# Optimization experiments

Measured on AMD Instinct MI355X. Metric: run time of the kernel, lower is better.

The kernel has to match this reference:

```python
import jax, jax.numpy as jnp
import numpy as np

B, S, D, T, H = 4, 2048, 1024, 5, 8


def setup_inputs() -> dict:
    key = jax.random.key(0)
    ks = jax.random.split(key, 12)
    sc = 0.02  # small init scale for weights so attention logits stay sane
    return {
        "x": jax.random.normal(ks[0], (B, S, D), jnp.float32),
        "time_steps": jax.random.randint(ks[1], (B, S), 0, T),
        "gamma": jnp.ones((T, D), jnp.float32),
        "beta": jax.random.normal(ks[2], (T, D), jnp.float32) * sc,
        "decay": jnp.ones((T,), jnp.float32),
        "shift_W": jax.random.normal(ks[3], (D, D), jnp.float32) * sc,
        "shift_b": jax.random.normal(ks[4], (D,), jnp.float32) * sc,
        "in_proj_W": jax.random.normal(ks[5], (3 * D, D), jnp.float32) * sc,
        "in_proj_b": jax.random.normal(ks[6], (3 * D,), jnp.float32) * sc,
        "out_proj_W": jax.random.normal(ks[7], (D, D), jnp.float32) * sc,
        "out_proj_b": jax.random.normal(ks[8], (D,), jnp.float32) * sc,
    }


def reference(x, time_steps, gamma, beta, decay, shift_W, shift_b,
              in_proj_W, in_proj_b, out_proj_W, out_proj_b):
    eps = 1e-5
    T_ = gamma.shape[0]
    b_, s_, d_ = x.shape
    hd = d_ // H

    # --- per-token indexed LayerNorm + decay (vectorized gather of norm params) ---
    idx = jnp.clip(time_steps, 0, T_ - 1)              # safe gather index [B,S]
    mu = jnp.mean(x, axis=-1, keepdims=True)
    var = jnp.mean(jnp.square(x - mu), axis=-1, keepdims=True)
    xn = (x - mu) * jax.lax.rsqrt(var + eps)           # [B,S,D]
    normed = (xn * gamma[idx] + beta[idx]) * decay[idx][..., None]
    x = jnp.where((time_steps < T_)[..., None], normed, x)

    # --- residual temporal shift (Linear) ---
    x = x + x @ shift_W.T + shift_b

    # --- torch-style MultiheadAttention(x, x, x), batch_first ---
    qkv = x @ in_proj_W.T + in_proj_b                  # [B,S,3D]
    q, k, v = jnp.split(qkv, 3, axis=-1)
    q = q.reshape(b_, s_, H, hd)
    k = k.reshape(b_, s_, H, hd)
    v = v.reshape(b_, s_, H, hd)
    scale = 1.0 / jnp.sqrt(jnp.asarray(hd, x.dtype))
    scores = jnp.einsum('bqhd,bkhd->bhqk', q, k) * scale   # [B,H,S,S]
    attn = jax.nn.softmax(scores, axis=-1)
    ctx = jnp.einsum('bhqk,bkhd->bqhd', attn, v).reshape(b_, s_, d_)
    attended = ctx @ out_proj_W.T + out_proj_b
    return x + attended
```

## Files before the change

kernel.cpp:

```cpp
#include <hip/hip_runtime.h>
#include <math.h>

#define B_ 4
#define S_ 2048
#define D_ 1024
#define T_ 5
#define H_ 8
#define HD_ 128
#define M_ (B_*S_)

typedef __bf16 bf16x8 __attribute__((ext_vector_type(8)));
typedef float  f32x4  __attribute__((ext_vector_type(4)));

__device__ __forceinline__ float bf2f(unsigned short u) {
    union { unsigned int i; float f; } c; c.i = ((unsigned int)u) << 16; return c.f;
}
__device__ __forceinline__ unsigned short f2bf(float f) {
    __bf16 h = (__bf16)f;
    unsigned short u; __builtin_memcpy(&u, &h, 2); return u;
}

__device__ __forceinline__ void gll16(const void* g, void* l) {
    __builtin_amdgcn_global_load_lds(
        (const __attribute__((address_space(1))) void*)g,
        (__attribute__((address_space(3))) void*)l, 16, 0, 0);
}

__global__ __launch_bounds__(256) void f2bf_kernel(
    const float* __restrict__ src, unsigned short* __restrict__ dst)
{
    int i = (blockIdx.x * 256 + threadIdx.x) * 4;
    float4 v = *(const float4*)(src + i);
    ushort4 o;
    o.x = f2bf(v.x); o.y = f2bf(v.y); o.z = f2bf(v.z); o.w = f2bf(v.w);
    *(ushort4*)(dst + i) = o;
}

__global__ __launch_bounds__(256) void ln_kernel(
    const float* __restrict__ x, const int* __restrict__ ts,
    const float* __restrict__ gamma, const float* __restrict__ beta,
    const float* __restrict__ decay, unsigned short* __restrict__ out)
{
    int row = blockIdx.x;
    int tid = threadIdx.x;
    float4 v = ((const float4*)(x + (size_t)row * D_))[tid];
    float s  = v.x + v.y + v.z + v.w;
    float s2 = v.x*v.x + v.y*v.y + v.z*v.z + v.w*v.w;
    #pragma unroll
    for (int off = 32; off; off >>= 1) {
        s  += __shfl_down(s,  off);
        s2 += __shfl_down(s2, off);
    }
    __shared__ float ps[4], ps2[4];
    if ((tid & 63) == 0) { ps[tid >> 6] = s; ps2[tid >> 6] = s2; }
    __syncthreads();
    float tot  = ps[0]  + ps[1]  + ps[2]  + ps[3];
    float tot2 = ps2[0] + ps2[1] + ps2[2] + ps2[3];
    float mu   = tot  * (1.0f / D_);
    float var  = tot2 * (1.0f / D_) - mu * mu;
    float rstd = rsqrtf(var + 1e-5f);

    int t  = ts[row];
    int tc = min(max(t, 0), T_ - 1);
    float4 g = ((const float4*)(gamma + (size_t)tc * D_))[tid];
    float4 b = ((const float4*)(beta  + (size_t)tc * D_))[tid];
    float dec = decay[tc];

    float4 o;
    o.x = ((v.x - mu) * rstd * g.x + b.x) * dec;
    o.y = ((v.y - mu) * rstd * g.y + b.y) * dec;
    o.z = ((v.z - mu) * rstd * g.z + b.z) * dec;
    o.w = ((v.w - mu) * rstd * g.w + b.w) * dec;
    if (t >= T_) o = v;
    ushort4 ob;
    ob.x = f2bf(o.x); ob.y = f2bf(o.y); ob.z = f2bf(o.z); ob.w = f2bf(o.w);
    ((ushort4*)(out + (size_t)row * D_))[tid] = ob;
}

__global__ __launch_bounds__(256) void gemm_mfma(
    const unsigned short* __restrict__ A,
    const unsigned short* __restrict__ Wt,
    const float* __restrict__ bias,
    const float* __restrict__ ResF,
    const unsigned short* __restrict__ ResB,
    float* __restrict__ Cf,
    unsigned short* __restrict__ Cb,
    int M, int N, int K)
{
    __shared__ __align__(16) unsigned short As[128 * 32];
    __shared__ __align__(16) unsigned short Bs[128 * 32];
    int tid  = threadIdx.x;
    int w    = tid >> 6, lane = tid & 63;
    int lm   = lane & 15, quad = lane >> 4;
    int wm   = w & 1,  wn   = w >> 1;
    int i0 = blockIdx.y * 128, j0 = blockIdx.x * 128;

    f32x4 acc[4][4];
    #pragma unroll
    for (int mt = 0; mt < 4; ++mt)
        #pragma unroll
        for (int nt = 0; nt < 4; ++nt)
            acc[mt][nt] = (f32x4){0.f, 0.f, 0.f, 0.f};

    int c0 = w * 128 + lane;
    int r0 = c0 >> 2,   k80 = (c0 & 3) * 8;
    int c1 = c0 + 64;
    int r1 = c1 >> 2,   k81 = (c1 & 3) * 8;

    for (int kt = 0; kt < K; kt += 32) {
        __syncthreads();
        gll16(A  + (size_t)(i0 + r0) * K + kt + k80, As + (size_t)(w * 128 + 0 ) * 8);
        gll16(A  + (size_t)(i0 + r1) * K + kt + k81, As + (size_t)(w * 128 + 64) * 8);
        gll16(Wt + (size_t)(j0 + r0) * K + kt + k80, Bs + (size_t)(w * 128 + 0 ) * 8);
        gll16(Wt + (size_t)(j0 + r1) * K + kt + k81, Bs + (size_t)(w * 128 + 64) * 8);
        __syncthreads();

        bf16x8 af[4], bfr[4];
        #pragma unroll
        for (int mt = 0; mt < 4; ++mt)
            af[mt] = *(const bf16x8*)&As[(wm * 64 + mt * 16 + lm) * 32 + quad * 8];
        #pragma unroll
        for (int nt = 0; nt < 4; ++nt)
            bfr[nt] = *(const bf16x8*)&Bs[(wn * 64 + nt * 16 + lm) * 32 + quad * 8];
        #pragma unroll
        for (int mt = 0; mt < 4; ++mt)
            #pragma unroll
            for (int nt = 0; nt < 4; ++nt)
                acc[mt][nt] = __builtin_amdgcn_mfma_f32_16x16x32_bf16(
                    af[mt], bfr[nt], acc[mt][nt], 0, 0, 0);
    }

    #pragma unroll
    for (int nt = 0; nt < 4; ++nt) {
        int j = j0 + wn * 64 + nt * 16 + lm;
        float bj = bias[j];
        #pragma unroll
        for (int mt = 0; mt < 4; ++mt) {
            #pragma unroll
            for (int r = 0; r < 4; ++r) {
                int i = i0 + wm * 64 + mt * 16 + quad * 4 + r;
                size_t off = (size_t)i * N + j;
                float v = acc[mt][nt][r] + bj;
                if (ResF) v += ResF[off];
                else if (ResB) v += bf2f(ResB[off]);
                if (Cf) Cf[off] = v;
                if (Cb) Cb[off] = f2bf(v);
            }
        }
    }
}

__global__ __launch_bounds__(256) void transpose_v(
    const unsigned short* __restrict__ qkv, unsigned short* __restrict__ vt)
{
    __shared__ unsigned short Ts[64][72];
    int t = threadIdx.x;
    int s0 = blockIdx.x * 64, c0 = blockIdx.y * 64, b = blockIdx.z;
    int r  = t >> 2, cg = (t & 3) * 16;
    const unsigned short* src =
        qkv + (size_t)(b * S_ + s0 + r) * (3 * D_) + 2 * D_ + c0 + cg;
    *(bf16x8*)&Ts[r][cg]     = *(const bf16x8*)(src);
    *(bf16x8*)&Ts[r][cg + 8] = *(const bf16x8*)(src + 8);
    __syncthreads();
    int dd = t >> 2, sg = (t & 3) * 16;
    unsigned short tmp[16];
    #pragma unroll
    for (int j = 0; j < 16; ++j) tmp[j] = Ts[sg + j][dd];
    unsigned short* dst = vt + ((size_t)b * D_ + c0 + dd) * S_ + s0 + sg;
    *(bf16x8*)dst       = *(bf16x8*)&tmp[0];
    *(bf16x8*)(dst + 8) = *(bf16x8*)&tmp[8];
}

__global__ __launch_bounds__(256, 2) void flash_mfma(
    const unsigned short* __restrict__ qkv,
    const unsigned short* __restrict__ vt,
    unsigned short* __restrict__ ctx)
{
    __shared__ __align__(16) unsigned short Ks [2][64 * 128];
    __shared__ __align__(16) unsigned short Vts[2][128 * 64];
    __shared__ __align__(16) unsigned short Ps [4][32 * 64];

    int tid  = threadIdx.x;
    int w    = tid >> 6, lane = tid & 63;
    int lm   = lane & 15, quad = lane >> 4;
    int qt = blockIdx.x, h = blockIdx.y, b = blockIdx.z;
    const int rs = 3 * D_;
    const float scale = 0.08838834764831844f * 1.4426950408889634f;
    size_t qbase  = (size_t)b * S_ * rs + (size_t)h * HD_;
    size_t kbase  = qbase + D_;
    size_t vtbase = ((size_t)b * H_ + h) * (size_t)HD_ * S_;
    int q0 = qt * 128 + w * 32;

    int krow0 = w * 4 + (lane >> 4);
    int kcolE = ((((lane & 15) * 16) ^ ((krow0 & 7) << 4)) >> 1);
    int vrow0 = w * 8 + (lane >> 3);
    int vcolE = ((((lane & 7)  * 16) ^ ((vrow0 & 7) << 4)) >> 1);

    const int rxor = (lm & 7) << 4;

    #pragma unroll
    for (int i = 0; i < 4; ++i) {
        gll16(qkv + kbase + (size_t)(krow0 + 16 * i) * rs + kcolE,
              &Ks[0][i * 2048 + w * 512]);
        gll16(vt  + vtbase + (size_t)(vrow0 + 32 * i) * S_ + vcolE,
              &Vts[0][i * 2048 + w * 512]);
    }

    bf16x8 qf[2][4];
    #pragma unroll
    for (int mt = 0; mt < 2; ++mt)
        #pragma unroll
        for (int kc = 0; kc < 4; ++kc) {
            bf16x8 raw = *(const bf16x8*)(
                qkv + qbase + (size_t)(q0 + mt * 16 + lm) * rs + kc * 32 + quad * 8);
            bf16x8 sc;
            #pragma unroll
            for (int j = 0; j < 8; ++j)
                sc[j] = (__bf16)((float)raw[j] * scale);
            qf[mt][kc] = sc;
        }

    f32x4 oacc[2][8];
    #pragma unroll
    for (int mt = 0; mt < 2; ++mt)
        #pragma unroll
        for (int n = 0; n < 8; ++n)
            oacc[mt][n] = (f32x4){0.f, 0.f, 0.f, 0.f};
    float lst[2][4];
    #pragma unroll
    for (int mt = 0; mt < 2; ++mt)
        #pragma unroll
        for (int r = 0; r < 4; ++r) lst[mt][r] = 0.f;

    int cur = 0;
    for (int kt = 0; kt < S_ / 64; ++kt) {
        __syncthreads();

        if (kt + 1 < S_ / 64) {
            int k0n = (kt + 1) * 64, nb = cur ^ 1;
            #pragma unroll
            for (int i = 0; i < 4; ++i) {
                gll16(qkv + kbase + (size_t)(k0n + krow0 + 16 * i) * rs + kcolE,
                      &Ks[nb][i * 2048 + w * 512]);
                gll16(vt  + vtbase + (size_t)(vrow0 + 32 * i) * S_ + k0n + vcolE,
                      &Vts[nb][i * 2048 + w * 512]);
            }
        }

        const char* Kb = (const char*)&Ks[cur][0];
        const char* Vb = (const char*)&Vts[cur][0];

        f32x4 sacc[2][4];
        #pragma unroll
        for (int mt = 0; mt < 2; ++mt)
            #pragma unroll
            for (int n = 0; n < 4; ++n)
                sacc[mt][n] = (f32x4){0.f, 0.f, 0.f, 0.f};
        __builtin_amdgcn_s_setprio(1);
        #pragma unroll
        for (int n = 0; n < 4; ++n) {
            bf16x8 bk[4];
            #pragma unroll
            for (int kc = 0; kc < 4; ++kc)
                bk[kc] = *(const bf16x8*)(Kb + (n * 16 + lm) * 256 +
                                          ((kc * 64 + quad * 16) ^ rxor));
            #pragma unroll
            for (int mt = 0; mt < 2; ++mt)
                #pragma unroll
                for (int kc = 0; kc < 4; ++kc)
                    sacc[mt][n] = __builtin_amdgcn_mfma_f32_16x16x32_bf16(
                        qf[mt][kc], bk[kc], sacc[mt][n], 0, 0, 0);
        }
        __builtin_amdgcn_s_setprio(0);

        char* Pw = (char*)&Ps[w][0];
        #pragma unroll
        for (int mt = 0; mt < 2; ++mt) {
            #pragma unroll
            for (int r = 0; r < 4; ++r) {
                float p0 = exp2f(sacc[mt][0][r]);
                float p1 = exp2f(sacc[mt][1][r]);
                float p2 = exp2f(sacc[mt][2][r]);
                float p3 = exp2f(sacc[mt][3][r]);
                lst[mt][r] += (p0 + p1) + (p2 + p3);
                int row = mt * 16 + quad * 4 + r;
                int wx  = (row & 7) << 4;
                char* rowp = Pw + row * 128;
                *(unsigned short*)(rowp + (( 0 + lm * 2) ^ wx)) = f2bf(p0);
                *(unsigned short*)(rowp + ((32 + lm * 2) ^ wx)) = f2bf(p1);
                *(unsigned short*)(rowp + ((64 + lm * 2) ^ wx)) = f2bf(p2);
                *(unsigned short*)(rowp + ((96 + lm * 2) ^ wx)) = f2bf(p3);
            }
        }

        bf16x8 pa[2][2];
        #pragma unroll
        for (int mt = 0; mt < 2; ++mt)
            #pragma unroll
            for (int kc = 0; kc < 2; ++kc)
                pa[mt][kc] = *(const bf16x8*)(Pw + (mt * 16 + lm) * 128 +
                                              ((kc * 64 + quad * 16) ^ rxor));
        __builtin_amdgcn_s_setprio(1);
        #pragma unroll
        for (int n = 0; n < 8; ++n) {
            bf16x8 bv0 = *(const bf16x8*)(Vb + (n * 16 + lm) * 128 +
                                          (( 0 + quad * 16) ^ rxor));
            bf16x8 bv1 = *(const bf16x8*)(Vb + (n * 16 + lm) * 128 +
                                          ((64 + quad * 16) ^ rxor));
            #pragma unroll
            for (int mt = 0; mt < 2; ++mt) {
                oacc[mt][n] = __builtin_amdgcn_mfma_f32_16x16x32_bf16(
                    pa[mt][0], bv0, oacc[mt][n], 0, 0, 0);
                oacc[mt][n] = __builtin_amdgcn_mfma_f32_16x16x32_bf16(
                    pa[mt][1], bv1, oacc[mt][n], 0, 0, 0);
            }
        }
        __builtin_amdgcn_s_setprio(0);
        cur ^= 1;
    }

    float linv[2][4];
    #pragma unroll
    for (int mt = 0; mt < 2; ++mt)
        #pragma unroll
        for (int r = 0; r < 4; ++r) {
            float l = lst[mt][r];
            l += __shfl_xor(l, 1);
            l += __shfl_xor(l, 2);
            l += __shfl_xor(l, 4);
            l += __shfl_xor(l, 8);
            linv[mt][r] = 1.0f / l;
        }
    size_t rowbase = (size_t)b * S_ + (size_t)qt * 128 + w * 32;
    #pragma unroll
    for (int mt = 0; mt < 2; ++mt)
        #pragma unroll
        for (int r = 0; r < 4; ++r) {
            size_t row = rowbase + mt * 16 + quad * 4 + r;
            unsigned short* dst = ctx + row * D_ + h * HD_ + lm;
            #pragma unroll
            for (int n = 0; n < 8; ++n)
                dst[n * 16] = f2bf(oacc[mt][n][r] * linv[mt][r]);
        }
}

extern "C" void kernel_launch(void* const* d_in, const int* in_sizes, int n_in,
                              void* d_out, int out_size, void* d_ws, size_t ws_size,
                              hipStream_t stream) {
    (void)in_sizes; (void)n_in; (void)out_size; (void)ws_size;
    const float* x          = (const float*)d_in[0];
    const int*   ts         = (const int*)  d_in[1];
    const float* gamma      = (const float*)d_in[2];
    const float* beta       = (const float*)d_in[3];
    const float* decay      = (const float*)d_in[4];
    const float* shift_W    = (const float*)d_in[5];
    const float* shift_b    = (const float*)d_in[6];
    const float* in_proj_W  = (const float*)d_in[7];
    const float* in_proj_b  = (const float*)d_in[8];
    const float* out_proj_W = (const float*)d_in[9];
    const float* out_proj_b = (const float*)d_in[10];
    float* out = (float*)d_out;

    unsigned short* p     = (unsigned short*)d_ws;
    unsigned short* xln_b = p;
    unsigned short* qkv_b = xln_b + (size_t)M_ * D_;
    unsigned short* xs_b  = qkv_b + (size_t)M_ * 3 * D_;
    unsigned short* wsh_b = xs_b  + (size_t)M_ * D_;
    unsigned short* wip_b = wsh_b + (size_t)D_ * D_;
    unsigned short* wop_b = wip_b + (size_t)3 * D_ * D_;
    unsigned short* vt_b  = xs_b;
    unsigned short* ctx_b = xln_b;
    float* xs = out;

    f2bf_kernel<<<D_ * D_ / 1024,     256, 0, stream>>>(shift_W,    wsh_b);
    f2bf_kernel<<<3 * D_ * D_ / 1024, 256, 0, stream>>>(in_proj_W,  wip_b);
    f2bf_kernel<<<D_ * D_ / 1024,     256, 0, stream>>>(out_proj_W, wop_b);

    ln_kernel<<<M_, 256, 0, stream>>>(x, ts, gamma, beta, decay, xln_b);

    gemm_mfma<<<dim3(D_ / 128, M_ / 128), 256, 0, stream>>>(
        xln_b, wsh_b, shift_b, nullptr, xln_b, xs, xs_b, M_, D_, D_);
    gemm_mfma<<<dim3(3 * D_ / 128, M_ / 128), 256, 0, stream>>>(
        xs_b, wip_b, in_proj_b, nullptr, nullptr, nullptr, qkv_b, M_, 3 * D_, D_);

    transpose_v<<<dim3(S_ / 64, D_ / 64, B_), 256, 0, stream>>>(qkv_b, vt_b);
    flash_mfma<<<dim3(S_ / 128, H_, B_), 256, 0, stream>>>(qkv_b, vt_b, ctx_b);

    gemm_mfma<<<dim3(D_ / 128, M_ / 128), 256, 0, stream>>>(
        ctx_b, wop_b, out_proj_b, xs, nullptr, out, nullptr, M_, D_, D_);
}
```

Measured before the change: 412.2 us.

## Merge weight conversions, swizzle GEMM block order, use fast exp in attention

Three weight-conversion launches become one kernel that dispatches on index, relying on the bf16 weight buffers being contiguous. The GEMM remaps linear block IDs across eight groups to change the tile scheduling order and improve cache locality. f2bf becomes a manual round-to-nearest-even bit trick, and flash attention switches from exp2f with a log2e-folded scale to __expf with the plain scale. These are several unrelated micro-changes; the exp change assumes __expf lowers to an exp2 plus multiply, so it may add an instruction rather than save one.

Result: faster. 392.8 us (-4.7%).

```diff
diff --git a/kernel.cpp b/kernel.cpp
--- a/kernel.cpp
+++ b/kernel.cpp
@@ -16,8 +16,10 @@
     union { unsigned int i; float f; } c; c.i = ((unsigned int)u) << 16; return c.f;
 }
 __device__ __forceinline__ unsigned short f2bf(float f) {
-    __bf16 h = (__bf16)f;
-    unsigned short u; __builtin_memcpy(&u, &h, 2); return u;
+    union { float f; unsigned int i; } c; c.f = f;
+    unsigned int u = c.i;
+    u += 0x7fffu + ((u >> 16) & 1u);
+    return (unsigned short)(u >> 16);
 }
 
 __device__ __forceinline__ void gll16(const void* g, void* l) {
@@ -26,11 +28,19 @@
         (__attribute__((address_space(3))) void*)l, 16, 0, 0);
 }
 
-__global__ __launch_bounds__(256) void f2bf_kernel(
-    const float* __restrict__ src, unsigned short* __restrict__ dst)
+__global__ __launch_bounds__(256) void f2bf3_kernel(
+    const float* __restrict__ s0,
+    const float* __restrict__ s1,
+    const float* __restrict__ s2,
+    unsigned short* __restrict__ dst)
 {
     int i = (blockIdx.x * 256 + threadIdx.x) * 4;
-    float4 v = *(const float4*)(src + i);
+    const float* src;
+    int local;
+    if (i < D_ * D_)              { src = s0; local = i; }
+    else if (i < 4 * D_ * D_)     { src = s1; local = i - D_ * D_; }
+    else                          { src = s2; local = i - 4 * D_ * D_; }
+    float4 v = *(const float4*)(src + local);
     ushort4 o;
     o.x = f2bf(v.x); o.y = f2bf(v.y); o.z = f2bf(v.z); o.w = f2bf(v.w);
     *(ushort4*)(dst + i) = o;
@@ -93,7 +103,14 @@
     int w    = tid >> 6, lane = tid & 63;
     int lm   = lane & 15, quad = lane >> 4;
     int wm   = w & 1,  wn   = w >> 1;
-    int i0 = blockIdx.y * 128, j0 = blockIdx.x * 128;
+
+    int nwgx  = gridDim.x;
+    int lin   = blockIdx.y * nwgx + blockIdx.x;
+    int chunk = (nwgx * gridDim.y) >> 3;
+    int swz   = (lin & 7) * chunk + (lin >> 3);
+    int bx    = swz % nwgx, by = swz / nwgx;
+
+    int i0 = by * 128, j0 = bx * 128;
 
     f32x4 acc[4][4];
     #pragma unroll
@@ -185,7 +202,7 @@
     int lm   = lane & 15, quad = lane >> 4;
     int qt = blockIdx.x, h = blockIdx.y, b = blockIdx.z;
     const int rs = 3 * D_;
-    const float scale = 0.08838834764831844f * 1.4426950408889634f;
+    const float scale = 0.08838834764831844f;
     size_t qbase  = (size_t)b * S_ * rs + (size_t)h * HD_;
     size_t kbase  = qbase + D_;
     size_t vtbase = ((size_t)b * H_ + h) * (size_t)HD_ * S_;
@@ -278,10 +295,10 @@
         for (int mt = 0; mt < 2; ++mt) {
             #pragma unroll
             for (int r = 0; r < 4; ++r) {
-                float p0 = exp2f(sacc[mt][0][r]);
-                float p1 = exp2f(sacc[mt][1][r]);
-                float p2 = exp2f(sacc[mt][2][r]);
-                float p3 = exp2f(sacc[mt][3][r]);
+                float p0 = __expf(sacc[mt][0][r]);
+                float p1 = __expf(sacc[mt][1][r]);
+                float p2 = __expf(sacc[mt][2][r]);
+                float p3 = __expf(sacc[mt][3][r]);
                 lst[mt][r] += (p0 + p1) + (p2 + p3);
                 int row = mt * 16 + quad * 4 + r;
                 int wx  = (row & 7) << 4;
@@ -372,9 +389,8 @@
     unsigned short* ctx_b = xln_b;
     float* xs = out;
 
-    f2bf_kernel<<<D_ * D_ / 1024,     256, 0, stream>>>(shift_W,    wsh_b);
-    f2bf_kernel<<<3 * D_ * D_ / 1024, 256, 0, stream>>>(in_proj_W,  wip_b);
-    f2bf_kernel<<<D_ * D_ / 1024,     256, 0, stream>>>(out_proj_W, wop_b);
+    f2bf3_kernel<<<5 * D_ * D_ / 1024, 256, 0, stream>>>(
+        shift_W, in_proj_W, out_proj_W, wsh_b);
 
     ln_kernel<<<M_, 256, 0, stream>>>(x, ts, gamma, beta, decay, xln_b);
 
```
